# Optimization experiments

Measured on AMD Instinct MI355X. Metric: run time of the kernel, lower is better.

## Reference

```python
import jax, jax.numpy as jnp
import numpy as np

L = 4          # decomposition_levels
PRUNE_Q = 0.4  # pruning_ratio


def haar_dwt2(img):
    a = img[:, 0::2, 0::2]; b = img[:, 0::2, 1::2]
    c = img[:, 1::2, 0::2]; d = img[:, 1::2, 1::2]
    cA = (a + b + c + d) * 0.5
    cH = (a - b + c - d) * 0.5
    cV = (a + b - c - d) * 0.5
    cD = (a - b - c + d) * 0.5
    return cA, cH, cV, cD


def haar_idwt2(cA, cH, cV, cD):
    # exact inverse of haar_dwt2: [B, h, w] -> [B, 2h, 2w]
    a = (cA + cH + cV + cD) * 0.5
    b = (cA - cH + cV - cD) * 0.5
    c = (cA + cH - cV - cD) * 0.5
    d = (cA - cH - cV + cD) * 0.5
    B, h, w = cA.shape
    top = jnp.stack([a, b], axis=-1).reshape(B, h, 2 * w)  # interleave cols
    bot = jnp.stack([c, d], axis=-1).reshape(B, h, 2 * w)
    return jnp.stack([top, bot], axis=2).reshape(B, 2 * h, 2 * w)  # interleave rows


def setup_inputs() -> dict:
    key = jax.random.key(0)
    k1, k2, k3 = jax.random.split(key, 3)
    B, in_dim, out_dim = 128, 4096, 4096
    x = jax.random.normal(k1, (B, in_dim), jnp.float32)
    base_weight = jax.random.normal(k2, (out_dim, in_dim), jnp.float32) * 0.02
    bias = jax.random.normal(k3, (out_dim,), jnp.float32) * 0.02
    scale_factors = jnp.ones((L, 4), jnp.float32)  # per-level, per-subband
    return {"x": x, "base_weight": base_weight, "bias": bias,
            "scale_factors": scale_factors}


def reference(x, base_weight, bias, scale_factors):
    B, in_dim = x.shape
    S = int(np.sqrt(in_dim))  # 64: each sample viewed as SxS image
    base_out = x @ base_weight.T  # [B, out_dim]

    # multi-level Haar analysis with per-level scaling + quantile pruning
    cA = x.reshape(B, S, S)
    levels = []
    for l in range(L):
        cA, cH, cV, cD = haar_dwt2(cA)
        co = jnp.stack([cA, cH, cV, cD], axis=1)  # [B, 4, h, w]
        co = co * scale_factors[l][None, :, None, None]
        ab = jnp.abs(co)
        thr = jnp.quantile(ab, PRUNE_Q, axis=-1, keepdims=True)
        co = co * (ab > thr).astype(co.dtype)
        levels.append(co)

    # synthesis from pruned coefficients
    rec = levels[-1][:, 0]  # coarsest pruned cA
    for l in range(L - 1, -1, -1):
        rec = haar_idwt2(rec, levels[l][:, 1], levels[l][:, 2], levels[l][:, 3])

    wavelet_out = rec.reshape(B, in_dim)  # out_dim == in_dim
    return base_out + wavelet_out + bias
```

## Files before the change

kernel.cpp:

```cpp
#include <hip/hip_runtime.h>
#include <hip/hip_bf16.h>

typedef __attribute__((ext_vector_type(8))) short bf16x8;
typedef __attribute__((ext_vector_type(4))) float f32x4;

__device__ __forceinline__ unsigned short f2bf(float f) {
  unsigned int u = __float_as_uint(f);
  u += 0x7FFFu + ((u >> 16) & 1u);
  return (unsigned short)(u >> 16);
}

__device__ __forceinline__ bf16x8 pack8(float4 lo, float4 hi) {
  union { unsigned int u[4]; bf16x8 v; } r;
  asm("v_cvt_pk_bf16_f32 %0, %1, %2" : "=v"(r.u[0]) : "v"(lo.x), "v"(lo.y));
  asm("v_cvt_pk_bf16_f32 %0, %1, %2" : "=v"(r.u[1]) : "v"(lo.z), "v"(lo.w));
  asm("v_cvt_pk_bf16_f32 %0, %1, %2" : "=v"(r.u[2]) : "v"(hi.x), "v"(hi.y));
  asm("v_cvt_pk_bf16_f32 %0, %1, %2" : "=v"(r.u[3]) : "v"(hi.z), "v"(hi.w));
  return r.v;
}

__device__ __forceinline__ void gload16(const void* g, void* l) {
  __builtin_amdgcn_global_load_lds(
      (const __attribute__((address_space(1))) void*)g,
      (__attribute__((address_space(3))) void*)l, 16, 0, 0);
}

__host__ __device__ constexpr int prOffset(int l) {
  return (l == 0) ? 0 : (l == 1) ? 3072 : (l == 2) ? 3840 : 4032;
}

template<int L>
__device__ __forceinline__ void level_fwd(float* cur, float* tmp, float* ab,
                                          float* pr, float* thrL, float* thrH,
                                          const float* __restrict__ scl, int tid) {
  constexpr int HALF = 32 >> L, LOG2 = 5 - L, HH = HALF * HALF, TOT = 4 * HH;
  constexpr int H = HALF * 2;
  constexpr float P = 0.4f * (float)(HALF - 1);
  constexpr int K = (int)P;
  constexpr float FRAC = P - (float)K;
  const float s0 = scl[4 * L + 0], s1 = scl[4 * L + 1];
  const float s2 = scl[4 * L + 2], s3 = scl[4 * L + 3];
  for (int e = tid; e < HH; e += 512) {
    const int i = e >> LOG2, j = e & (HALF - 1);
    const float a = cur[(i * 2) * H + j * 2];
    const float b = cur[(i * 2) * H + j * 2 + 1];
    const float c = cur[(i * 2 + 1) * H + j * 2];
    const float d = cur[(i * 2 + 1) * H + j * 2 + 1];
    const float vA = (((a + b) + c) + d) * 0.5f;
    const float vH = (((a - b) + c) - d) * 0.5f;
    const float vV = (((a + b) - c) - d) * 0.5f;
    const float vD = (((a - b) - c) + d) * 0.5f;
    tmp[e]          = vA;  ab[e]          = fabsf(vA * s0);
    tmp[HH + e]     = vH;  ab[HH + e]     = fabsf(vH * s1);
    tmp[2 * HH + e] = vV;  ab[2 * HH + e] = fabsf(vV * s2);
    tmp[3 * HH + e] = vD;  ab[3 * HH + e] = fabsf(vD * s3);
  }
  __syncthreads();
  constexpr int CH = (TOT >= 512) ? TOT / 512 : 1;
  {
    const int base = tid * CH;
    if (base < TOT) {
      const int rowbase = base & ~(HALF - 1);
      float v[CH]; int clt[CH], ceq[CH];
#pragma unroll
      for (int c = 0; c < CH; ++c) { v[c] = ab[base + c]; clt[c] = 0; ceq[c] = 0; }
#pragma unroll
      for (int rr = 0; rr < HALF; ++rr) {
        const float a = ab[rowbase + rr];
#pragma unroll
        for (int c = 0; c < CH; ++c) {
          clt[c] += (a < v[c]) ? 1 : 0;
          ceq[c] += (a == v[c]) ? 1 : 0;
        }
      }
      const int row = base >> LOG2;
#pragma unroll
      for (int c = 0; c < CH; ++c) {
        if (clt[c] <= K && K < clt[c] + ceq[c]) thrL[row] = v[c];
        if (clt[c] <= K + 1 && K + 1 < clt[c] + ceq[c]) thrH[row] = v[c];
      }
    }
  }
  __syncthreads();
  for (int e = tid; e < TOT; e += 512) {
    const int s = e >> (2 * LOG2);
    const int row = e >> LOG2;
    const float sc = (s < 2) ? (s == 0 ? s0 : s1) : (s == 2 ? s2 : s3);
    const float thr = thrL[row] * (1.0f - FRAC) + thrH[row] * FRAC;
    const float co = tmp[e] * sc;
    const float val = (fabsf(co) > thr) ? co : 0.0f;
    if (s >= 1) pr[prOffset(L) + e - HH] = val;
    else {
      if (L == 3) pr[4080 + e] = val;
      cur[e] = tmp[e];
    }
  }
  __syncthreads();
}

__global__ __launch_bounds__(512) void wavelet_kernel(
    const float* __restrict__ x, const float* __restrict__ bias,
    const float* __restrict__ scl, float* __restrict__ out,
    unsigned short* __restrict__ xb, int writeXb) {
  __shared__ float sh[16384];
  float* cur = sh;
  float* tmp = sh + 4096;
  float* ab  = sh + 8192;
  float* pr  = sh + 12288;
  float* thrL = cur + 2048;
  float* thrH = cur + 2176;
  const int b = blockIdx.x, tid = threadIdx.x;
  const float* xi = x + (size_t)b * 4096;

  for (int i = tid; i < 1024; i += 512) {
    const float4 v = ((const float4*)xi)[i];
    *(float4*)&cur[i * 4] = v;
    if (writeXb) {
      ushort4 pk = {f2bf(v.x), f2bf(v.y), f2bf(v.z), f2bf(v.w)};
      *(ushort4*)&xb[(size_t)b * 4096 + i * 4] = pk;
    }
  }
  __syncthreads();

  level_fwd<0>(cur, tmp, ab, pr, thrL, thrH, scl, tid);
  level_fwd<1>(cur, tmp, ab, pr, thrL, thrH, scl, tid);
  level_fwd<2>(cur, tmp, ab, pr, thrL, thrH, scl, tid);
  level_fwd<3>(cur, tmp, ab, pr, thrL, thrH, scl, tid);

#pragma unroll
  for (int l = 3; l >= 0; --l) {
    const int half = 64 >> (l + 1);
    const int hh = half * half;
    const int po = prOffset(l);
    const float* src = (l == 3) ? &pr[4080] : ((l & 1) ? tmp : cur);
    float* dst = (l & 1) ? cur : tmp;
    const int W2 = half * 2;
    for (int e = tid; e < hh; e += 512) {
      const int i = e / half, j = e - i * half;
      const float cA = src[e];
      const float cH = pr[po + 0 * hh + i * half + j];
      const float cV = pr[po + 1 * hh + i * half + j];
      const float cD = pr[po + 2 * hh + i * half + j];
      const float a2 = (((cA + cH) + cV) + cD) * 0.5f;
      const float b2 = (((cA - cH) + cV) - cD) * 0.5f;
      const float c2 = (((cA + cH) - cV) - cD) * 0.5f;
      const float d2 = (((cA - cH) - cV) + cD) * 0.5f;
      dst[(i * 2) * W2 + j * 2]         = a2;
      dst[(i * 2) * W2 + j * 2 + 1]     = b2;
      dst[(i * 2 + 1) * W2 + j * 2]     = c2;
      dst[(i * 2 + 1) * W2 + j * 2 + 1] = d2;
    }
    __syncthreads();
  }
  float* o = out + (size_t)b * 4096;
  const float4* t4 = (const float4*)tmp;
  const float4* b4 = (const float4*)bias;
  for (int i = tid; i < 1024; i += 512) {
    float4 t = t4[i], bb = b4[i];
    float4 r = {t.x + bb.x, t.y + bb.y, t.z + bb.z, t.w + bb.w};
    ((float4*)o)[i] = r;
  }
}

__global__ __launch_bounds__(256, 4) void gemm_v4(
    const unsigned short* __restrict__ xb, const float* __restrict__ w,
    float* __restrict__ out) {
  __shared__ __align__(16) unsigned short A_lds[2][128 * 32];
  __shared__ __align__(16) float B_lds[2][64 * 32];
  const int tid = threadIdx.x, lane = tid & 63, wv = tid >> 6;
  const int fr = lane & 15, kq = lane >> 4;
  const int nt = blockIdx.x & 63, ks = blockIdx.x >> 6;
  const int n0 = nt * 64, k0 = ks * 256;

  const int sA0 = tid, sA1 = 256 + tid;
  const int rA0 = sA0 >> 2, cA0 = (sA0 & 3) ^ ((rA0 >> 1) & 3);
  const int rA1 = sA1 >> 2, cA1 = (sA1 & 3) ^ ((rA1 >> 1) & 3);
  const unsigned short* aSrc0 = xb + (size_t)rA0 * 4096 + k0 + cA0 * 8;
  const unsigned short* aSrc1 = xb + (size_t)rA1 * 4096 + k0 + cA1 * 8;
  const int rB0 = sA0 >> 3, cB0 = (sA0 & 7) ^ (rB0 & 7);
  const int rB1 = sA1 >> 3, cB1 = (sA1 & 7) ^ (rB1 & 7);
  const float* bSrc0 = w + (size_t)(n0 + rB0) * 4096 + k0 + cB0 * 4;
  const float* bSrc1 = w + (size_t)(n0 + rB1) * 4096 + k0 + cB1 * 4;

  f32x4 acc[8];
#pragma unroll
  for (int mi = 0; mi < 8; ++mi) acc[mi] = f32x4{0.f, 0.f, 0.f, 0.f};

  const int aslot = kq ^ ((fr >> 1) & 3);
  const int R2 = wv * 16 + fr;
  const int bo0 = R2 * 128 + (((kq * 2 + 0) ^ (R2 & 7)) * 16);
  const int bo1 = R2 * 128 + (((kq * 2 + 1) ^ (R2 & 7)) * 16);

  auto STAGE = [&](int buf, int t) {
    gload16(aSrc0 + t * 32, (char*)&A_lds[buf][0] + tid * 16);
    gload16(aSrc1 + t * 32, (char*)&A_lds[buf][0] + (256 + tid) * 16);
    gload16(bSrc0 + t * 32, (char*)&B_lds[buf][0] + tid * 16);
    gload16(bSrc1 + t * 32, (char*)&B_lds[buf][0] + (256 + tid) * 16);
  };

  STAGE(0, 0);
  __syncthreads();
  int cur = 0;
#pragma unroll
  for (int t = 0; t < 8; ++t) {
    if (t < 7) STAGE(cur ^ 1, t + 1);
    const char* Ab = (const char*)&A_lds[cur][0];
    const char* Bb = (const char*)&B_lds[cur][0];
    const float4 b0 = *(const float4*)(Bb + bo0);
    const float4 b1 = *(const float4*)(Bb + bo1);
    const bf16x8 bb = pack8(b0, b1);
#pragma unroll
    for (int mi = 0; mi < 8; ++mi) {
      const bf16x8 af = *(const bf16x8*)(Ab + (mi * 16 + fr) * 64 + aslot * 16);
      acc[mi] = __builtin_amdgcn_mfma_f32_16x16x32_bf16(af, bb, acc[mi], 0, 0, 0);
    }
    __syncthreads();
    cur ^= 1;
  }

  const int col = n0 + wv * 16 + fr;
  const int rq = kq * 4;
#pragma unroll
  for (int mi = 0; mi < 8; ++mi)
#pragma unroll
    for (int j = 0; j < 4; ++j)
      atomicAdd(&out[(size_t)(mi * 16 + rq + j) * 4096 + col], acc[mi][j]);
}

__global__ __launch_bounds__(256, 2) void gemm_kernel(
    const float* __restrict__ x, const float* __restrict__ w,
    float* __restrict__ out) {
  __shared__ __align__(16) unsigned short Asm[2][128][40];
  __shared__ __align__(16) unsigned short Bsm[2][64][40];
  const int tid = threadIdx.x;
  const int nt = blockIdx.x & 63, ks = blockIdx.x >> 6;
  const int n0 = nt * 64, k0 = ks * 512;
  const int q = tid & 7, r0 = tid >> 3;
  const int lane = tid & 63, wid = tid >> 6;
  const int wm = wid >> 1, wn = wid & 1;
  const int fr = lane & 15, k8 = (lane >> 4) * 8;

  f32x4 acc[4][2];
#pragma unroll
  for (int mi = 0; mi < 4; ++mi)
#pragma unroll
    for (int ni = 0; ni < 2; ++ni) acc[mi][ni] = f32x4{0.f, 0.f, 0.f, 0.f};

  float4 ra[4]; float4 rb[2];
#pragma unroll
  for (int p = 0; p < 4; ++p)
    ra[p] = *(const float4*)&x[(size_t)(r0 + p * 32) * 4096 + k0 + q * 4];
#pragma unroll
  for (int p = 0; p < 2; ++p)
    rb[p] = *(const float4*)&w[(size_t)(n0 + r0 + p * 32) * 4096 + k0 + q * 4];
#pragma unroll
  for (int p = 0; p < 4; ++p) {
    ushort4 pk = {f2bf(ra[p].x), f2bf(ra[p].y), f2bf(ra[p].z), f2bf(ra[p].w)};
    *(ushort4*)&Asm[0][r0 + p * 32][q * 4] = pk;
  }
#pragma unroll
  for (int p = 0; p < 2; ++p) {
    ushort4 pk = {f2bf(rb[p].x), f2bf(rb[p].y), f2bf(rb[p].z), f2bf(rb[p].w)};
    *(ushort4*)&Bsm[0][r0 + p * 32][q * 4] = pk;
  }
  __syncthreads();

  for (int t = 0; t < 16; ++t) {
    const int cb = t & 1;
    if (t < 15) {
      const int kg = k0 + (t + 1) * 32;
#pragma unroll
      for (int p = 0; p < 4; ++p)
        ra[p] = *(const float4*)&x[(size_t)(r0 + p * 32) * 4096 + kg + q * 4];
#pragma unroll
      for (int p = 0; p < 2; ++p)
        rb[p] = *(const float4*)&w[(size_t)(n0 + r0 + p * 32) * 4096 + kg + q * 4];
    }
    bf16x8 af[4], bg[2];
#pragma unroll
    for (int mi = 0; mi < 4; ++mi)
      af[mi] = *(const bf16x8*)&Asm[cb][wm * 64 + mi * 16 + fr][k8];
#pragma unroll
    for (int ni = 0; ni < 2; ++ni)
      bg[ni] = *(const bf16x8*)&Bsm[cb][wn * 32 + ni * 16 + fr][k8];
#pragma unroll
    for (int mi = 0; mi < 4; ++mi)
#pragma unroll
      for (int ni = 0; ni < 2; ++ni)
        acc[mi][ni] = __builtin_amdgcn_mfma_f32_16x16x32_bf16(af[mi], bg[ni],
                                                              acc[mi][ni], 0, 0, 0);
    if (t < 15) {
#pragma unroll
      for (int p = 0; p < 4; ++p) {
        ushort4 pk = {f2bf(ra[p].x), f2bf(ra[p].y), f2bf(ra[p].z), f2bf(ra[p].w)};
        *(ushort4*)&Asm[cb ^ 1][r0 + p * 32][q * 4] = pk;
      }
#pragma unroll
      for (int p = 0; p < 2; ++p) {
        ushort4 pk = {f2bf(rb[p].x), f2bf(rb[p].y), f2bf(rb[p].z), f2bf(rb[p].w)};
        *(ushort4*)&Bsm[cb ^ 1][r0 + p * 32][q * 4] = pk;
      }
    }
    __syncthreads();
  }

  const int rbase = wm * 64 + (lane >> 4) * 4;
  const int cbase = n0 + wn * 32 + fr;
#pragma unroll
  for (int mi = 0; mi < 4; ++mi)
#pragma unroll
    for (int ni = 0; ni < 2; ++ni)
#pragma unroll
      for (int j = 0; j < 4; ++j)
        atomicAdd(&out[(size_t)(rbase + mi * 16 + j) * 4096 + cbase + ni * 16],
                  acc[mi][ni][j]);
}

extern "C" void kernel_launch(void* const* d_in, const int* in_sizes, int n_in,
                              void* d_out, int out_size, void* d_ws, size_t ws_size,
                              hipStream_t stream) {
  const float* x    = (const float*)d_in[0];
  const float* w    = (const float*)d_in[1];
  const float* bias = (const float*)d_in[2];
  const float* scl  = (const float*)d_in[3];
  float* out = (float*)d_out;
  const bool useWs = ws_size >= (size_t)128 * 4096 * 2;
  unsigned short* xbp = (unsigned short*)d_ws;
  hipLaunchKernelGGL(wavelet_kernel, dim3(128), dim3(512), 0, stream,
                     x, bias, scl, out, xbp, useWs ? 1 : 0);
  if (useWs)
    hipLaunchKernelGGL(gemm_v4, dim3(1024), dim3(256), 0, stream, xbp, w, out);
  else
    hipLaunchKernelGGL(gemm_kernel, dim3(512), dim3(256), 0, stream, x, w, out);
}
```

Baseline: 135.6 us.

## Replace atomic split-K GEMM with partial-sum buffers reduced in wavelet epilogue

Adds a new path used when the workspace is large enough. A separate kernel converts x to bf16. A split-K GEMM over 8 K-slices of 512 writes plain partial sums to a workspace buffer instead of issuing atomicAdd into the output. The wavelet kernel then runs last and adds the 8 partials plus bias while writing the output. This removes atomic contention and the ordering dependency on the wavelet kernel, at the cost of an extra launch and 16 MB of partial writes and reads.

```diff
diff --git a/kernel.cpp b/kernel.cpp
--- a/kernel.cpp
+++ b/kernel.cpp
@@ -27,6 +27,14 @@
 
 __host__ __device__ constexpr int prOffset(int l) {
   return (l == 0) ? 0 : (l == 1) ? 3072 : (l == 2) ? 3840 : 4032;
+}
+
+__global__ __launch_bounds__(256) void cvt_x(const float* __restrict__ x,
+                                             unsigned short* __restrict__ xb) {
+  const int i = blockIdx.x * 256 + threadIdx.x;
+  const float4 v = ((const float4*)x)[i];
+  ushort4 pk = {f2bf(v.x), f2bf(v.y), f2bf(v.z), f2bf(v.w)};
+  ((ushort4*)xb)[i] = pk;
 }
 
 template<int L>
@@ -101,7 +109,8 @@
 __global__ __launch_bounds__(512) void wavelet_kernel(
     const float* __restrict__ x, const float* __restrict__ bias,
     const float* __restrict__ scl, float* __restrict__ out,
-    unsigned short* __restrict__ xb, int writeXb) {
+    unsigned short* __restrict__ xb, const float* __restrict__ partials,
+    int writeXb, int addPartials) {
   __shared__ float sh[16384];
   float* cur = sh;
   float* tmp = sh + 4096;
@@ -157,9 +166,83 @@
   const float4* b4 = (const float4*)bias;
   for (int i = tid; i < 1024; i += 512) {
     float4 t = t4[i], bb = b4[i];
-    float4 r = {t.x + bb.x, t.y + bb.y, t.z + bb.z, t.w + bb.w};
-    ((float4*)o)[i] = r;
-  }
+    float4 s = {t.x + bb.x, t.y + bb.y, t.z + bb.z, t.w + bb.w};
+    if (addPartials) {
+#pragma unroll
+      for (int ks = 0; ks < 8; ++ks) {
+        const float4 p = *(const float4*)&partials[(size_t)ks * 524288 +
+                                                   (size_t)b * 4096 + i * 4];
+        s.x += p.x; s.y += p.y; s.z += p.z; s.w += p.w;
+      }
+    }
+    ((float4*)o)[i] = s;
+  }
+}
+
+__global__ __launch_bounds__(256, 4) void gemm_v5(
+    const unsigned short* __restrict__ xb, const float* __restrict__ w,
+    float* __restrict__ partials) {
+  __shared__ __align__(16) unsigned short A_lds[2][128 * 32];
+  __shared__ __align__(16) float B_lds[2][64 * 32];
+  const int tid = threadIdx.x, lane = tid & 63, wv = tid >> 6;
+  const int fr = lane & 15, kq = lane >> 4;
+  const int nt = blockIdx.x & 63, ks = blockIdx.x >> 6;
+  const int n0 = nt * 64, k0 = ks * 512;
+
+  const int sA0 = tid, sA1 = 256 + tid;
+  const int rA0 = sA0 >> 2, cA0 = (sA0 & 3) ^ ((rA0 >> 1) & 3);
+  const int rA1 = sA1 >> 2, cA1 = (sA1 & 3) ^ ((rA1 >> 1) & 3);
+  const unsigned short* aSrc0 = xb + (size_t)rA0 * 4096 + k0 + cA0 * 8;
+  const unsigned short* aSrc1 = xb + (size_t)rA1 * 4096 + k0 + cA1 * 8;
+  const int rB0 = sA0 >> 3, cB0 = (sA0 & 7) ^ (rB0 & 7);
+  const int rB1 = sA1 >> 3, cB1 = (sA1 & 7) ^ (rB1 & 7);
+  const float* bSrc0 = w + (size_t)(n0 + rB0) * 4096 + k0 + cB0 * 4;
+  const float* bSrc1 = w + (size_t)(n0 + rB1) * 4096 + k0 + cB1 * 4;
+
+  f32x4 acc[8];
+#pragma unroll
+  for (int mi = 0; mi < 8; ++mi) acc[mi] = f32x4{0.f, 0.f, 0.f, 0.f};
+
+  const int aslot = kq ^ ((fr >> 1) & 3);
+  const int R2 = wv * 16 + fr;
+  const int bo0 = R2 * 128 + (((kq * 2 + 0) ^ (R2 & 7)) * 16);
+  const int bo1 = R2 * 128 + (((kq * 2 + 1) ^ (R2 & 7)) * 16);
+
+  auto STAGE = [&](int buf, int t) {
+    gload16(aSrc0 + t * 32, (char*)&A_lds[buf][0] + tid * 16);
+    gload16(aSrc1 + t * 32, (char*)&A_lds[buf][0] + (256 + tid) * 16);
+    gload16(bSrc0 + t * 32, (char*)&B_lds[buf][0] + tid * 16);
+    gload16(bSrc1 + t * 32, (char*)&B_lds[buf][0] + (256 + tid) * 16);
+  };
+
+  STAGE(0, 0);
+  __syncthreads();
+  int cur = 0;
+#pragma unroll
+  for (int t = 0; t < 16; ++t) {
+    if (t < 15) STAGE(cur ^ 1, t + 1);
+    const char* Ab = (const char*)&A_lds[cur][0];
+    const char* Bb = (const char*)&B_lds[cur][0];
+    const float4 b0 = *(const float4*)(Bb + bo0);
+    const float4 b1 = *(const float4*)(Bb + bo1);
+    const bf16x8 bb = pack8(b0, b1);
+#pragma unroll
+    for (int mi = 0; mi < 8; ++mi) {
+      const bf16x8 af = *(const bf16x8*)(Ab + (mi * 16 + fr) * 64 + aslot * 16);
+      acc[mi] = __builtin_amdgcn_mfma_f32_16x16x32_bf16(af, bb, acc[mi], 0, 0, 0);
+    }
+    __syncthreads();
+    cur ^= 1;
+  }
+
+  float* P = partials + (size_t)ks * 524288;
+  const int col = n0 + wv * 16 + fr;
+  const int rq = kq * 4;
+#pragma unroll
+  for (int mi = 0; mi < 8; ++mi)
+#pragma unroll
+    for (int j = 0; j < 4; ++j)
+      P[(size_t)(mi * 16 + rq + j) * 4096 + col] = acc[mi][j];
 }
 
 __global__ __launch_bounds__(256, 4) void gemm_v4(
@@ -324,12 +407,24 @@
   const float* bias = (const float*)d_in[2];
   const float* scl  = (const float*)d_in[3];
   float* out = (float*)d_out;
-  const bool useWs = ws_size >= (size_t)128 * 4096 * 2;
   unsigned short* xbp = (unsigned short*)d_ws;
-  hipLaunchKernelGGL(wavelet_kernel, dim3(128), dim3(512), 0, stream,
-                     x, bias, scl, out, xbp, useWs ? 1 : 0);
-  if (useWs)
+  float* partials = (float*)((char*)d_ws + (1 << 20));
+  const size_t needFull = (1u << 20) + 8u * 524288u * 4u;
+  const bool fullWs = ws_size >= needFull;
+  const bool miniWs = ws_size >= (size_t)128 * 4096 * 2;
+
+  if (fullWs) {
+    hipLaunchKernelGGL(cvt_x, dim3(512), dim3(256), 0, stream, x, xbp);
+    hipLaunchKernelGGL(gemm_v5, dim3(512), dim3(256), 0, stream, xbp, w, partials);
+    hipLaunchKernelGGL(wavelet_kernel, dim3(128), dim3(512), 0, stream,
+                       x, bias, scl, out, xbp, partials, 0, 1);
+  } else if (miniWs) {
+    hipLaunchKernelGGL(wavelet_kernel, dim3(128), dim3(512), 0, stream,
+                       x, bias, scl, out, xbp, (const float*)nullptr, 1, 0);
     hipLaunchKernelGGL(gemm_v4, dim3(1024), dim3(256), 0, stream, xbp, w, out);
-  else
+  } else {
+    hipLaunchKernelGGL(wavelet_kernel, dim3(128), dim3(512), 0, stream,
+                       x, bias, scl, out, xbp, (const float*)nullptr, 0, 0);
     hipLaunchKernelGGL(gemm_kernel, dim3(512), dim3(256), 0, stream, x, w, out);
-}
+  }
+}
```

After: 127.8 us. 5.8% less time.

## Co-schedule wavelet and GEMM blocks in one kernel with split-K partials

Applied to the files above, without the earlier changes.

The x-to-bf16 conversion moves into its own small kernel. The wavelet blocks and GEMM blocks then run concurrently inside a single fused kernel, so the wavelet work overlaps the GEMM instead of serialising before it. The GEMM now uses 512-thread blocks with a 1024-wide K slice and 4 split-K slices, writing plain stores to a partials buffer instead of issuing atomics. A reduce kernel then adds the partials into the output. The quantile search pads the abs buffer rows and reads them as float4, which adds two extra launches and extra partials traffic in exchange.

```diff
diff --git a/kernel.cpp b/kernel.cpp
--- a/kernel.cpp
+++ b/kernel.cpp
@@ -29,12 +29,21 @@
   return (l == 0) ? 0 : (l == 1) ? 3072 : (l == 2) ? 3840 : 4032;
 }
 
+__global__ __launch_bounds__(256) void cvt_x(const float* __restrict__ x,
+                                             unsigned short* __restrict__ xb) {
+  const int i = blockIdx.x * 256 + threadIdx.x;
+  const float4 v = ((const float4*)x)[i];
+  ushort4 pk = {f2bf(v.x), f2bf(v.y), f2bf(v.z), f2bf(v.w)};
+  ((ushort4*)xb)[i] = pk;
+}
+
 template<int L>
 __device__ __forceinline__ void level_fwd(float* cur, float* tmp, float* ab,
                                           float* pr, float* thrL, float* thrH,
                                           const float* __restrict__ scl, int tid) {
   constexpr int HALF = 32 >> L, LOG2 = 5 - L, HH = HALF * HALF, TOT = 4 * HH;
   constexpr int H = HALF * 2;
+  constexpr int ST = HALF + 4;
   constexpr float P = 0.4f * (float)(HALF - 1);
   constexpr int K = (int)P;
   constexpr float FRAC = P - (float)K;
@@ -50,30 +59,35 @@
     const float vH = (((a - b) + c) - d) * 0.5f;
     const float vV = (((a + b) - c) - d) * 0.5f;
     const float vD = (((a - b) - c) + d) * 0.5f;
-    tmp[e]          = vA;  ab[e]          = fabsf(vA * s0);
-    tmp[HH + e]     = vH;  ab[HH + e]     = fabsf(vH * s1);
-    tmp[2 * HH + e] = vV;  ab[2 * HH + e] = fabsf(vV * s2);
-    tmp[3 * HH + e] = vD;  ab[3 * HH + e] = fabsf(vD * s3);
+    tmp[e]          = vA;  ab[(0 * HALF + i) * ST + j] = fabsf(vA * s0);
+    tmp[HH + e]     = vH;  ab[(1 * HALF + i) * ST + j] = fabsf(vH * s1);
+    tmp[2 * HH + e] = vV;  ab[(2 * HALF + i) * ST + j] = fabsf(vV * s2);
+    tmp[3 * HH + e] = vD;  ab[(3 * HALF + i) * ST + j] = fabsf(vD * s3);
   }
   __syncthreads();
   constexpr int CH = (TOT >= 512) ? TOT / 512 : 1;
   {
     const int base = tid * CH;
     if (base < TOT) {
-      const int rowbase = base & ~(HALF - 1);
+      const int row = base >> LOG2;
+      const int c0 = base & (HALF - 1);
+      const float* rp = &ab[row * ST];
       float v[CH]; int clt[CH], ceq[CH];
 #pragma unroll
-      for (int c = 0; c < CH; ++c) { v[c] = ab[base + c]; clt[c] = 0; ceq[c] = 0; }
-#pragma unroll
-      for (int rr = 0; rr < HALF; ++rr) {
-        const float a = ab[rowbase + rr];
-#pragma unroll
-        for (int c = 0; c < CH; ++c) {
-          clt[c] += (a < v[c]) ? 1 : 0;
-          ceq[c] += (a == v[c]) ? 1 : 0;
+      for (int c = 0; c < CH; ++c) { v[c] = rp[c0 + c]; clt[c] = 0; ceq[c] = 0; }
+#pragma unroll
+      for (int rq = 0; rq < HALF / 4; ++rq) {
+        const float4 q = *(const float4*)&rp[rq * 4];
+        float qa[4] = {q.x, q.y, q.z, q.w};
+#pragma unroll
+        for (int z = 0; z < 4; ++z) {
+#pragma unroll
+          for (int c = 0; c < CH; ++c) {
+            clt[c] += (qa[z] < v[c]) ? 1 : 0;
+            ceq[c] += (qa[z] == v[c]) ? 1 : 0;
+          }
         }
       }
-      const int row = base >> LOG2;
 #pragma unroll
       for (int c = 0; c < CH; ++c) {
         if (clt[c] <= K && K < clt[c] + ceq[c]) thrL[row] = v[c];
@@ -98,28 +112,18 @@
   __syncthreads();
 }
 
-__global__ __launch_bounds__(512) void wavelet_kernel(
-    const float* __restrict__ x, const float* __restrict__ bias,
-    const float* __restrict__ scl, float* __restrict__ out,
-    unsigned short* __restrict__ xb, int writeXb) {
-  __shared__ float sh[16384];
+__device__ __forceinline__ void wavelet_block(
+    float* sh, const float* __restrict__ x, const float* __restrict__ bias,
+    const float* __restrict__ scl, float* __restrict__ out, int b, int tid) {
   float* cur = sh;
   float* tmp = sh + 4096;
   float* ab  = sh + 8192;
   float* pr  = sh + 12288;
   float* thrL = cur + 2048;
   float* thrH = cur + 2176;
-  const int b = blockIdx.x, tid = threadIdx.x;
   const float* xi = x + (size_t)b * 4096;
-
-  for (int i = tid; i < 1024; i += 512) {
-    const float4 v = ((const float4*)xi)[i];
-    *(float4*)&cur[i * 4] = v;
-    if (writeXb) {
-      ushort4 pk = {f2bf(v.x), f2bf(v.y), f2bf(v.z), f2bf(v.w)};
-      *(ushort4*)&xb[(size_t)b * 4096 + i * 4] = pk;
-    }
-  }
+  for (int i = tid; i < 1024; i += 512)
+    *(float4*)&cur[i * 4] = ((const float4*)xi)[i];
   __syncthreads();
 
   level_fwd<0>(cur, tmp, ab, pr, thrL, thrH, scl, tid);
@@ -162,69 +166,95 @@
   }
 }
 
-__global__ __launch_bounds__(256, 4) void gemm_v4(
-    const unsigned short* __restrict__ xb, const float* __restrict__ w,
-    float* __restrict__ out) {
-  __shared__ __align__(16) unsigned short A_lds[2][128 * 32];
-  __shared__ __align__(16) float B_lds[2][64 * 32];
+__device__ __forceinline__ void gemm_block(
+    char* smem, int gb, const unsigned short* __restrict__ xb,
+    const float* __restrict__ w, float* __restrict__ partials) {
+  unsigned short* Abuf = (unsigned short*)smem;
+  char* Bbuf = smem + 16384;
   const int tid = threadIdx.x, lane = tid & 63, wv = tid >> 6;
   const int fr = lane & 15, kq = lane >> 4;
-  const int nt = blockIdx.x & 63, ks = blockIdx.x >> 6;
-  const int n0 = nt * 64, k0 = ks * 256;
-
-  const int sA0 = tid, sA1 = 256 + tid;
-  const int rA0 = sA0 >> 2, cA0 = (sA0 & 3) ^ ((rA0 >> 1) & 3);
-  const int rA1 = sA1 >> 2, cA1 = (sA1 & 3) ^ ((rA1 >> 1) & 3);
-  const unsigned short* aSrc0 = xb + (size_t)rA0 * 4096 + k0 + cA0 * 8;
-  const unsigned short* aSrc1 = xb + (size_t)rA1 * 4096 + k0 + cA1 * 8;
-  const int rB0 = sA0 >> 3, cB0 = (sA0 & 7) ^ (rB0 & 7);
-  const int rB1 = sA1 >> 3, cB1 = (sA1 & 7) ^ (rB1 & 7);
-  const float* bSrc0 = w + (size_t)(n0 + rB0) * 4096 + k0 + cB0 * 4;
-  const float* bSrc1 = w + (size_t)(n0 + rB1) * 4096 + k0 + cB1 * 4;
-
-  f32x4 acc[8];
-#pragma unroll
-  for (int mi = 0; mi < 8; ++mi) acc[mi] = f32x4{0.f, 0.f, 0.f, 0.f};
-
-  const int aslot = kq ^ ((fr >> 1) & 3);
-  const int R2 = wv * 16 + fr;
-  const int bo0 = R2 * 128 + (((kq * 2 + 0) ^ (R2 & 7)) * 16);
-  const int bo1 = R2 * 128 + (((kq * 2 + 1) ^ (R2 & 7)) * 16);
+  const int nt = gb & 63, ks = gb >> 6;
+  const int n0 = nt * 64, k0 = ks * 1024;
+
+  const int ra = tid >> 2, ca = (tid & 3) ^ ((ra >> 1) & 3);
+  const unsigned short* aSrc = xb + (size_t)ra * 4096 + k0 + ca * 8;
+  const int rb = tid >> 3, cb = (tid & 7) ^ (rb & 7);
+  const float* bSrc = w + (size_t)(n0 + rb) * 4096 + k0 + cb * 4;
+  char* aDst = (char*)Abuf + tid * 16;
+  char* bDst = Bbuf + tid * 16;
+
+  const int asw = (fr >> 1) & 3, bsw = fr & 7;
+  const int RB = (wv & 3) * 16 + fr;
+  const int bo0 = RB * 128 + (((2 * kq) ^ bsw) << 4);
+  const int bo1 = RB * 128 + (((2 * kq + 1) ^ bsw) << 4);
+  const int aoBase = ((wv >> 2) * 64 + fr) * 64 + ((kq ^ asw) << 4);
+
+  f32x4 acc[4];
+#pragma unroll
+  for (int mi = 0; mi < 4; ++mi) acc[mi] = f32x4{0.f, 0.f, 0.f, 0.f};
 
   auto STAGE = [&](int buf, int t) {
-    gload16(aSrc0 + t * 32, (char*)&A_lds[buf][0] + tid * 16);
-    gload16(aSrc1 + t * 32, (char*)&A_lds[buf][0] + (256 + tid) * 16);
-    gload16(bSrc0 + t * 32, (char*)&B_lds[buf][0] + tid * 16);
-    gload16(bSrc1 + t * 32, (char*)&B_lds[buf][0] + (256 + tid) * 16);
+    gload16(aSrc + t * 32, aDst + buf * 8192);
+    gload16(bSrc + t * 32, bDst + buf * 8192);
   };
 
   STAGE(0, 0);
   __syncthreads();
-  int cur = 0;
-#pragma unroll
-  for (int t = 0; t < 8; ++t) {
-    if (t < 7) STAGE(cur ^ 1, t + 1);
-    const char* Ab = (const char*)&A_lds[cur][0];
-    const char* Bb = (const char*)&B_lds[cur][0];
-    const float4 b0 = *(const float4*)(Bb + bo0);
-    const float4 b1 = *(const float4*)(Bb + bo1);
-    const bf16x8 bb = pack8(b0, b1);
-#pragma unroll
-    for (int mi = 0; mi < 8; ++mi) {
-      const bf16x8 af = *(const bf16x8*)(Ab + (mi * 16 + fr) * 64 + aslot * 16);
-      acc[mi] = __builtin_amdgcn_mfma_f32_16x16x32_bf16(af, bb, acc[mi], 0, 0, 0);
+  for (int t = 0; t < 32; ++t) {
+    const int cur = t & 1;
+    if (t < 31) STAGE(cur ^ 1, t + 1);
+    const char* A = (const char*)Abuf + cur * 8192;
+    const char* B = Bbuf + cur * 8192;
+    const float4 b0 = *(const float4*)(B + bo0);
+    const float4 b1 = *(const float4*)(B + bo1);
+    const bf16x8 bbv = pack8(b0, b1);
+#pragma unroll
+    for (int mi = 0; mi < 4; ++mi) {
+      const bf16x8 af = *(const bf16x8*)(A + aoBase + mi * 1024);
+      acc[mi] = __builtin_amdgcn_mfma_f32_16x16x32_bf16(af, bbv, acc[mi], 0, 0, 0);
     }
     __syncthreads();
-    cur ^= 1;
-  }
-
-  const int col = n0 + wv * 16 + fr;
-  const int rq = kq * 4;
-#pragma unroll
-  for (int mi = 0; mi < 8; ++mi)
+  }
+
+  float* P = partials + (size_t)ks * 524288;
+  const int col = n0 + (wv & 3) * 16 + fr;
+  const int r0 = (wv >> 2) * 64 + kq * 4;
+#pragma unroll
+  for (int mi = 0; mi < 4; ++mi)
 #pragma unroll
     for (int j = 0; j < 4; ++j)
-      atomicAdd(&out[(size_t)(mi * 16 + rq + j) * 4096 + col], acc[mi][j]);
+      P[(size_t)(r0 + mi * 16 + j) * 4096 + col] = acc[mi][j];
+}
+
+__global__ __launch_bounds__(512, 4) void fused_kernel(
+    const float* __restrict__ x, const float* __restrict__ bias,
+    const float* __restrict__ scl, float* __restrict__ out,
+    const unsigned short* __restrict__ xb, const float* __restrict__ w,
+    float* __restrict__ partials) {
+  __shared__ __align__(16) float sh[16384];
+  if (blockIdx.x < 128)
+    wavelet_block(sh, x, bias, scl, out, blockIdx.x, threadIdx.x);
+  else
+    gemm_block((char*)sh, blockIdx.x - 128, xb, w, partials);
+}
+
+__global__ __launch_bounds__(256) void reduce_k(float* __restrict__ out,
+                                                const float* __restrict__ partials) {
+  const int i = blockIdx.x * 256 + threadIdx.x;
+  float4 o = ((float4*)out)[i];
+#pragma unroll
+  for (int ks = 0; ks < 4; ++ks) {
+    const float4 p = ((const float4*)(partials + (size_t)ks * 524288))[i];
+    o.x += p.x; o.y += p.y; o.z += p.z; o.w += p.w;
+  }
+  ((float4*)out)[i] = o;
+}
+
+__global__ __launch_bounds__(512) void wavelet_only(
+    const float* __restrict__ x, const float* __restrict__ bias,
+    const float* __restrict__ scl, float* __restrict__ out) {
+  __shared__ __align__(16) float sh[16384];
+  wavelet_block(sh, x, bias, scl, out, blockIdx.x, threadIdx.x);
 }
 
 __global__ __launch_bounds__(256, 2) void gemm_kernel(
@@ -266,7 +296,7 @@
   __syncthreads();
 
   for (int t = 0; t < 16; ++t) {
-    const int cb = t & 1;
+    const int cb2 = t & 1;
     if (t < 15) {
       const int kg = k0 + (t + 1) * 32;
 #pragma unroll
@@ -279,10 +309,10 @@
     bf16x8 af[4], bg[2];
 #pragma unroll
     for (int mi = 0; mi < 4; ++mi)
-      af[mi] = *(const bf16x8*)&Asm[cb][wm * 64 + mi * 16 + fr][k8];
+      af[mi] = *(const bf16x8*)&Asm[cb2][wm * 64 + mi * 16 + fr][k8];
 #pragma unroll
     for (int ni = 0; ni < 2; ++ni)
-      bg[ni] = *(const bf16x8*)&Bsm[cb][wn * 32 + ni * 16 + fr][k8];
+      bg[ni] = *(const bf16x8*)&Bsm[cb2][wn * 32 + ni * 16 + fr][k8];
 #pragma unroll
     for (int mi = 0; mi < 4; ++mi)
 #pragma unroll
@@ -293,12 +323,12 @@
 #pragma unroll
       for (int p = 0; p < 4; ++p) {
         ushort4 pk = {f2bf(ra[p].x), f2bf(ra[p].y), f2bf(ra[p].z), f2bf(ra[p].w)};
-        *(ushort4*)&Asm[cb ^ 1][r0 + p * 32][q * 4] = pk;
+        *(ushort4*)&Asm[cb2 ^ 1][r0 + p * 32][q * 4] = pk;
       }
 #pragma unroll
       for (int p = 0; p < 2; ++p) {
         ushort4 pk = {f2bf(rb[p].x), f2bf(rb[p].y), f2bf(rb[p].z), f2bf(rb[p].w)};
-        *(ushort4*)&Bsm[cb ^ 1][r0 + p * 32][q * 4] = pk;
+        *(ushort4*)&Bsm[cb2 ^ 1][r0 + p * 32][q * 4] = pk;
       }
     }
     __syncthreads();
@@ -324,12 +354,17 @@
   const float* bias = (const float*)d_in[2];
   const float* scl  = (const float*)d_in[3];
   float* out = (float*)d_out;
-  const bool useWs = ws_size >= (size_t)128 * 4096 * 2;
   unsigned short* xbp = (unsigned short*)d_ws;
-  hipLaunchKernelGGL(wavelet_kernel, dim3(128), dim3(512), 0, stream,
-                     x, bias, scl, out, xbp, useWs ? 1 : 0);
-  if (useWs)
-    hipLaunchKernelGGL(gemm_v4, dim3(1024), dim3(256), 0, stream, xbp, w, out);
-  else
+  float* partials = (float*)((char*)d_ws + (1 << 20));
+  const size_t need = (1u << 20) + 4u * 524288u * 4u;
+  if (ws_size >= need) {
+    hipLaunchKernelGGL(cvt_x, dim3(512), dim3(256), 0, stream, x, xbp);
+    hipLaunchKernelGGL(fused_kernel, dim3(384), dim3(512), 0, stream,
+                       x, bias, scl, out, xbp, w, partials);
+    hipLaunchKernelGGL(reduce_k, dim3(512), dim3(256), 0, stream, out, partials);
+  } else {
+    hipLaunchKernelGGL(wavelet_only, dim3(128), dim3(512), 0, stream,
+                       x, bias, scl, out);
     hipLaunchKernelGGL(gemm_kernel, dim3(512), dim3(256), 0, stream, x, w, out);
-}
+  }
+}
```

Result: faster. 126.4 us (-6.8%).

## Replace GEMM atomics with split-K partials reduced in the wavelet epilogue

Applied to the files above, without the earlier changes.

Reorders the pipeline: a small kernel converts x to bf16, the GEMM uses split-K of 8 (512-deep) and writes per-split partials without atomics, and the wavelet kernel runs last and sums the partials plus bias into the output. The wavelet kernel moves to 1024 threads, and its quantile rank-count buffer gets padded rows read as float4 to cut LDS bank conflicts and load count. This removes atomic traffic, but adds a 16 MB partials round trip and an extra launch, and the wavelet stage now sits serially after the GEMM.

```diff
diff --git a/kernel.cpp b/kernel.cpp
--- a/kernel.cpp
+++ b/kernel.cpp
@@ -29,18 +29,27 @@
   return (l == 0) ? 0 : (l == 1) ? 3072 : (l == 2) ? 3840 : 4032;
 }
 
+__global__ __launch_bounds__(256) void cvt_x(const float* __restrict__ x,
+                                             unsigned short* __restrict__ xb) {
+  const int i = blockIdx.x * 256 + threadIdx.x;
+  const float4 v = ((const float4*)x)[i];
+  ushort4 pk = {f2bf(v.x), f2bf(v.y), f2bf(v.z), f2bf(v.w)};
+  ((ushort4*)xb)[i] = pk;
+}
+
 template<int L>
 __device__ __forceinline__ void level_fwd(float* cur, float* tmp, float* ab,
                                           float* pr, float* thrL, float* thrH,
                                           const float* __restrict__ scl, int tid) {
   constexpr int HALF = 32 >> L, LOG2 = 5 - L, HH = HALF * HALF, TOT = 4 * HH;
   constexpr int H = HALF * 2;
+  constexpr int ST = HALF + 4;
   constexpr float P = 0.4f * (float)(HALF - 1);
   constexpr int K = (int)P;
   constexpr float FRAC = P - (float)K;
   const float s0 = scl[4 * L + 0], s1 = scl[4 * L + 1];
   const float s2 = scl[4 * L + 2], s3 = scl[4 * L + 3];
-  for (int e = tid; e < HH; e += 512) {
+  for (int e = tid; e < HH; e += 1024) {
     const int i = e >> LOG2, j = e & (HALF - 1);
     const float a = cur[(i * 2) * H + j * 2];
     const float b = cur[(i * 2) * H + j * 2 + 1];
@@ -50,30 +59,35 @@
     const float vH = (((a - b) + c) - d) * 0.5f;
     const float vV = (((a + b) - c) - d) * 0.5f;
     const float vD = (((a - b) - c) + d) * 0.5f;
-    tmp[e]          = vA;  ab[e]          = fabsf(vA * s0);
-    tmp[HH + e]     = vH;  ab[HH + e]     = fabsf(vH * s1);
-    tmp[2 * HH + e] = vV;  ab[2 * HH + e] = fabsf(vV * s2);
-    tmp[3 * HH + e] = vD;  ab[3 * HH + e] = fabsf(vD * s3);
-  }
-  __syncthreads();
-  constexpr int CH = (TOT >= 512) ? TOT / 512 : 1;
+    tmp[e]          = vA;  ab[(0 * HALF + i) * ST + j] = fabsf(vA * s0);
+    tmp[HH + e]     = vH;  ab[(1 * HALF + i) * ST + j] = fabsf(vH * s1);
+    tmp[2 * HH + e] = vV;  ab[(2 * HALF + i) * ST + j] = fabsf(vV * s2);
+    tmp[3 * HH + e] = vD;  ab[(3 * HALF + i) * ST + j] = fabsf(vD * s3);
+  }
+  __syncthreads();
+  constexpr int CH = (TOT >= 1024) ? TOT / 1024 : 1;
   {
     const int base = tid * CH;
     if (base < TOT) {
-      const int rowbase = base & ~(HALF - 1);
+      const int row = base >> LOG2;
+      const int c0 = base & (HALF - 1);
+      const float* rp = &ab[row * ST];
       float v[CH]; int clt[CH], ceq[CH];
 #pragma unroll
-      for (int c = 0; c < CH; ++c) { v[c] = ab[base + c]; clt[c] = 0; ceq[c] = 0; }
-#pragma unroll
-      for (int rr = 0; rr < HALF; ++rr) {
-        const float a = ab[rowbase + rr];
-#pragma unroll
-        for (int c = 0; c < CH; ++c) {
-          clt[c] += (a < v[c]) ? 1 : 0;
-          ceq[c] += (a == v[c]) ? 1 : 0;
+      for (int c = 0; c < CH; ++c) { v[c] = rp[c0 + c]; clt[c] = 0; ceq[c] = 0; }
+#pragma unroll
+      for (int rq = 0; rq < HALF / 4; ++rq) {
+        const float4 q = *(const float4*)&rp[rq * 4];
+        float qa[4] = {q.x, q.y, q.z, q.w};
+#pragma unroll
+        for (int z = 0; z < 4; ++z) {
+#pragma unroll
+          for (int c = 0; c < CH; ++c) {
+            clt[c] += (qa[z] < v[c]) ? 1 : 0;
+            ceq[c] += (qa[z] == v[c]) ? 1 : 0;
+          }
         }
       }
-      const int row = base >> LOG2;
 #pragma unroll
       for (int c = 0; c < CH; ++c) {
         if (clt[c] <= K && K < clt[c] + ceq[c]) thrL[row] = v[c];
@@ -82,7 +96,7 @@
     }
   }
   __syncthreads();
-  for (int e = tid; e < TOT; e += 512) {
+  for (int e = tid; e < TOT; e += 1024) {
     const int s = e >> (2 * LOG2);
     const int row = e >> LOG2;
     const float sc = (s < 2) ? (s == 0 ? s0 : s1) : (s == 2 ? s2 : s3);
@@ -98,11 +112,11 @@
   __syncthreads();
 }
 
-__global__ __launch_bounds__(512) void wavelet_kernel(
+__global__ __launch_bounds__(1024) void wavelet_kernel(
     const float* __restrict__ x, const float* __restrict__ bias,
     const float* __restrict__ scl, float* __restrict__ out,
-    unsigned short* __restrict__ xb, int writeXb) {
-  __shared__ float sh[16384];
+    const float* __restrict__ partials, int addPartials) {
+  __shared__ __align__(16) float sh[16384];
   float* cur = sh;
   float* tmp = sh + 4096;
   float* ab  = sh + 8192;
@@ -112,14 +126,8 @@
   const int b = blockIdx.x, tid = threadIdx.x;
   const float* xi = x + (size_t)b * 4096;
 
-  for (int i = tid; i < 1024; i += 512) {
-    const float4 v = ((const float4*)xi)[i];
-    *(float4*)&cur[i * 4] = v;
-    if (writeXb) {
-      ushort4 pk = {f2bf(v.x), f2bf(v.y), f2bf(v.z), f2bf(v.w)};
-      *(ushort4*)&xb[(size_t)b * 4096 + i * 4] = pk;
-    }
-  }
+  for (int i = tid; i < 1024; i += 1024)
+    *(float4*)&cur[i * 4] = ((const float4*)xi)[i];
   __syncthreads();
 
   level_fwd<0>(cur, tmp, ab, pr, thrL, thrH, scl, tid);
@@ -135,7 +143,7 @@
     const float* src = (l == 3) ? &pr[4080] : ((l & 1) ? tmp : cur);
     float* dst = (l & 1) ? cur : tmp;
     const int W2 = half * 2;
-    for (int e = tid; e < hh; e += 512) {
+    for (int e = tid; e < hh; e += 1024) {
       const int i = e / half, j = e - i * half;
       const float cA = src[e];
       const float cH = pr[po + 0 * hh + i * half + j];
@@ -155,22 +163,30 @@
   float* o = out + (size_t)b * 4096;
   const float4* t4 = (const float4*)tmp;
   const float4* b4 = (const float4*)bias;
-  for (int i = tid; i < 1024; i += 512) {
+  for (int i = tid; i < 1024; i += 1024) {
     float4 t = t4[i], bb = b4[i];
-    float4 r = {t.x + bb.x, t.y + bb.y, t.z + bb.z, t.w + bb.w};
-    ((float4*)o)[i] = r;
-  }
-}
-
-__global__ __launch_bounds__(256, 4) void gemm_v4(
+    float4 s = {t.x + bb.x, t.y + bb.y, t.z + bb.z, t.w + bb.w};
+    if (addPartials) {
+#pragma unroll
+      for (int ks = 0; ks < 8; ++ks) {
+        const float4 p = *(const float4*)&partials[(size_t)ks * 524288 +
+                                                   (size_t)b * 4096 + i * 4];
+        s.x += p.x; s.y += p.y; s.z += p.z; s.w += p.w;
+      }
+    }
+    ((float4*)o)[i] = s;
+  }
+}
+
+__global__ __launch_bounds__(256, 4) void gemm_v5(
     const unsigned short* __restrict__ xb, const float* __restrict__ w,
-    float* __restrict__ out) {
+    float* __restrict__ partials) {
   __shared__ __align__(16) unsigned short A_lds[2][128 * 32];
   __shared__ __align__(16) float B_lds[2][64 * 32];
   const int tid = threadIdx.x, lane = tid & 63, wv = tid >> 6;
   const int fr = lane & 15, kq = lane >> 4;
   const int nt = blockIdx.x & 63, ks = blockIdx.x >> 6;
-  const int n0 = nt * 64, k0 = ks * 256;
+  const int n0 = nt * 64, k0 = ks * 512;
 
   const int sA0 = tid, sA1 = 256 + tid;
   const int rA0 = sA0 >> 2, cA0 = (sA0 & 3) ^ ((rA0 >> 1) & 3);
@@ -202,8 +218,8 @@
   __syncthreads();
   int cur = 0;
 #pragma unroll
-  for (int t = 0; t < 8; ++t) {
-    if (t < 7) STAGE(cur ^ 1, t + 1);
+  for (int t = 0; t < 16; ++t) {
+    if (t < 15) STAGE(cur ^ 1, t + 1);
     const char* Ab = (const char*)&A_lds[cur][0];
     const char* Bb = (const char*)&B_lds[cur][0];
     const float4 b0 = *(const float4*)(Bb + bo0);
@@ -218,13 +234,14 @@
     cur ^= 1;
   }
 
+  float* P = partials + (size_t)ks * 524288;
   const int col = n0 + wv * 16 + fr;
   const int rq = kq * 4;
 #pragma unroll
   for (int mi = 0; mi < 8; ++mi)
 #pragma unroll
     for (int j = 0; j < 4; ++j)
-      atomicAdd(&out[(size_t)(mi * 16 + rq + j) * 4096 + col], acc[mi][j]);
+      P[(size_t)(mi * 16 + rq + j) * 4096 + col] = acc[mi][j];
 }
 
 __global__ __launch_bounds__(256, 2) void gemm_kernel(
@@ -266,7 +283,7 @@
   __syncthreads();
 
   for (int t = 0; t < 16; ++t) {
-    const int cb = t & 1;
+    const int cb2 = t & 1;
     if (t < 15) {
       const int kg = k0 + (t + 1) * 32;
 #pragma unroll
@@ -279,10 +296,10 @@
     bf16x8 af[4], bg[2];
 #pragma unroll
     for (int mi = 0; mi < 4; ++mi)
-      af[mi] = *(const bf16x8*)&Asm[cb][wm * 64 + mi * 16 + fr][k8];
+      af[mi] = *(const bf16x8*)&Asm[cb2][wm * 64 + mi * 16 + fr][k8];
 #pragma unroll
     for (int ni = 0; ni < 2; ++ni)
-      bg[ni] = *(const bf16x8*)&Bsm[cb][wn * 32 + ni * 16 + fr][k8];
+      bg[ni] = *(const bf16x8*)&Bsm[cb2][wn * 32 + ni * 16 + fr][k8];
 #pragma unroll
     for (int mi = 0; mi < 4; ++mi)
 #pragma unroll
@@ -293,12 +310,12 @@
 #pragma unroll
       for (int p = 0; p < 4; ++p) {
         ushort4 pk = {f2bf(ra[p].x), f2bf(ra[p].y), f2bf(ra[p].z), f2bf(ra[p].w)};
-        *(ushort4*)&Asm[cb ^ 1][r0 + p * 32][q * 4] = pk;
+        *(ushort4*)&Asm[cb2 ^ 1][r0 + p * 32][q * 4] = pk;
       }
 #pragma unroll
       for (int p = 0; p < 2; ++p) {
         ushort4 pk = {f2bf(rb[p].x), f2bf(rb[p].y), f2bf(rb[p].z), f2bf(rb[p].w)};
-        *(ushort4*)&Bsm[cb ^ 1][r0 + p * 32][q * 4] = pk;
+        *(ushort4*)&Bsm[cb2 ^ 1][r0 + p * 32][q * 4] = pk;
       }
     }
     __syncthreads();
@@ -324,12 +341,17 @@
   const float* bias = (const float*)d_in[2];
   const float* scl  = (const float*)d_in[3];
   float* out = (float*)d_out;
-  const bool useWs = ws_size >= (size_t)128 * 4096 * 2;
   unsigned short* xbp = (unsigned short*)d_ws;
-  hipLaunchKernelGGL(wavelet_kernel, dim3(128), dim3(512), 0, stream,
-                     x, bias, scl, out, xbp, useWs ? 1 : 0);
-  if (useWs)
-    hipLaunchKernelGGL(gemm_v4, dim3(1024), dim3(256), 0, stream, xbp, w, out);
-  else
+  float* partials = (float*)((char*)d_ws + (1 << 20));
+  const size_t need = (1u << 20) + 8u * 524288u * 4u;
+  if (ws_size >= need) {
+    hipLaunchKernelGGL(cvt_x, dim3(512), dim3(256), 0, stream, x, xbp);
+    hipLaunchKernelGGL(gemm_v5, dim3(512), dim3(256), 0, stream, xbp, w, partials);
+    hipLaunchKernelGGL(wavelet_kernel, dim3(128), dim3(1024), 0, stream,
+                       x, bias, scl, out, partials, 1);
+  } else {
+    hipLaunchKernelGGL(wavelet_kernel, dim3(128), dim3(1024), 0, stream,
+                       x, bias, scl, out, (const float*)nullptr, 0);
     hipLaunchKernelGGL(gemm_kernel, dim3(512), dim3(256), 0, stream, x, w, out);
-}
+  }
+}
```

After: 126.0 us. -7.1%, faster.
